# Performance work log

Measured on AMD Instinct MI355X. Metric: run time of the kernel, lower is better.

## Reference

```python
import jax, jax.numpy as jnp
import numpy as np

MAX_DEGREE = 5
NUM_LAYERS = 2


def setup_inputs() -> dict:
    key = jax.random.key(0)
    ks = jax.random.split(key, 10)
    N, F, H, C, E = 200000, 128, 64, 40, 3200000
    x = jax.random.normal(ks[0], (N, F), dtype=jnp.float32)
    edge_index = jax.random.randint(ks[1], (2, E), 0, N, dtype=jnp.int32)
    # torch Linear init ~ U(-1/sqrt(fan_in), 1/sqrt(fan_in)); scaled normals are fine for a baseline
    W1 = jax.random.normal(ks[2], (F, H), dtype=jnp.float32) / np.sqrt(F)
    b1 = jax.random.normal(ks[3], (H,), dtype=jnp.float32) * 0.01
    relW = jax.random.normal(ks[4], (NUM_LAYERS, MAX_DEGREE + 1, H, H), dtype=jnp.float32) / np.sqrt(H)
    relb = jax.random.normal(ks[5], (NUM_LAYERS, MAX_DEGREE + 1, H), dtype=jnp.float32) * 0.01
    Wout = jax.random.normal(ks[6], (H, C), dtype=jnp.float32) / np.sqrt(H)
    bout = jax.random.normal(ks[7], (C,), dtype=jnp.float32) * 0.01
    fuse = jnp.full((NUM_LAYERS,), 1.0 / (NUM_LAYERS + 1), dtype=jnp.float32)
    return {"x": x, "edge_index": edge_index, "W1": W1, "b1": b1,
            "relW": relW, "relb": relb, "Wout": Wout, "bout": bout, "fuse": fuse}


def reference(x, edge_index, W1, b1, relW, relb, Wout, bout, fuse):
    N = x.shape[0]
    src, dst = edge_index[0], edge_index[1]
    loop_mask = (src != dst)  # remove_self_loops
    # degree on target nodes (flow='source_to_target'), clamped to max_degree
    deg = jax.ops.segment_sum(loop_mask.astype(jnp.int32), dst, num_segments=N)
    deg = jnp.clip(deg, 0, MAX_DEGREE)
    node_idx = jnp.arange(N)

    h = jax.nn.relu(x @ W1 + b1)  # dropout is identity in eval mode
    x_first = h
    for i in range(NUM_LAYERS):
        # scatter-add aggregation; self loops added back (root_weight=False)
        msg = jnp.where(loop_mask[:, None], h[src], 0.0)  # [E, H]
        agg = jax.ops.segment_sum(msg, dst, num_segments=N) + h  # [N, H]
        # degree-bucketed linear: compute all 6 buckets, select per node
        all_out = jnp.einsum('nd,kdo->kno', agg, relW[i]) + relb[i][:, None, :]  # [6, N, H]
        conv = all_out[deg, node_idx]  # [N, H]
        h = conv + fuse[i] * x_first
    logits = h @ Wout + bout
    return jax.nn.log_softmax(logits, axis=-1)
```

## Files before the change

kernel.cpp:

```cpp
#include <hip/hip_runtime.h>
#include <cmath>
#include <cstddef>

#define F_IN 128
#define H_DIM 64
#define C_OUT 40
#define MAXDEG 5
#define EPB 16

typedef __attribute__((ext_vector_type(8))) _Float16 half8;
typedef __attribute__((ext_vector_type(4))) _Float16 half4;
typedef __attribute__((ext_vector_type(4))) float fv4;
typedef __attribute__((ext_vector_type(2))) float fv2;

__device__ __forceinline__ half4 u2h(uint2 u) { return __builtin_bit_cast(half4, u); }
__device__ __forceinline__ uint2 h2u(half4 v) { return __builtin_bit_cast(uint2, v); }
__device__ __forceinline__ half8 u2h8(uint4 u) { return __builtin_bit_cast(half8, u); }
__device__ __forceinline__ uint4 h2u8(half8 v) { return __builtin_bit_cast(uint4, v); }


__global__ __launch_bounds__(256) void k_scatter(const int* __restrict__ src,
                                                 const int* __restrict__ dst,
                                                 int E, int NB, int stride,
                                                 int* __restrict__ gcnt,
                                                 unsigned int* __restrict__ ebuf) {
    __shared__ int hist[512];
    __shared__ int base[512];
    int tid = threadIdx.x;
    for (int i = tid; i < NB; i += 256) hist[i] = 0;
    __syncthreads();
    int e0 = blockIdx.x * (256 * EPB);
    int es[EPB], ed[EPB];
#pragma unroll
    for (int i = 0; i < EPB; ++i) {
        int e = e0 + i * 256 + tid;
        int s = -1, d = -1;
        if (e < E) { s = src[e]; d = dst[e]; }
        es[i] = s; ed[i] = d;
        if (d >= 0 && s != d) atomicAdd(&hist[d >> 9], 1);
    }
    __syncthreads();
    for (int i = tid; i < NB; i += 256) {
        int c = hist[i];
        base[i] = c ? atomicAdd(&gcnt[i], c) : 0;
        hist[i] = 0;
    }
    __syncthreads();
#pragma unroll
    for (int i = 0; i < EPB; ++i) {
        int s = es[i], d = ed[i];
        if (d >= 0 && s != d) {
            int b = d >> 9;
            int p = base[b] + atomicAdd(&hist[b], 1);
            if (p < stride)
                ebuf[(size_t)b * stride + p] = ((unsigned)(d & 511) << 20) | (unsigned)s;
        }
    }
}

__global__ __launch_bounds__(512) void k_build(const unsigned int* __restrict__ ebuf,
                                               const int* __restrict__ gcnt, int stride, int N,
                                               int* __restrict__ row, int* __restrict__ cnt,
                                               int* __restrict__ col) {
    __shared__ int lcnt[512];
    __shared__ int lcur[512];
    int bk = blockIdx.x;
    int n0 = bk << 9;
    int tid = threadIdx.x;
    int ebase = bk * stride;
    int ec = min(gcnt[bk], stride);
    int eend = ebase + ec;
    lcnt[tid] = 0;
    __syncthreads();
    for (int e = ebase + tid; e < eend; e += 512)
        atomicAdd(&lcnt[ebuf[e] >> 20], 1);
    __syncthreads();
    int v = lcnt[tid];
    lcur[tid] = v;
    __syncthreads();
    for (int off = 1; off < 512; off <<= 1) {
        int t = (tid >= off) ? lcur[tid - off] : 0;
        __syncthreads();
        lcur[tid] += t;
        __syncthreads();
    }
    int ex = lcur[tid] - v;
    __syncthreads();
    lcur[tid] = ebase + ex;
    int n = n0 + tid;
    if (n < N) {
        row[n] = ebase + ex;
        cnt[n] = v;
    }
    __syncthreads();
    for (int e = ebase + tid; e < eend; e += 512) {
        unsigned edv = ebuf[e];
        int dl = edv >> 20;
        int p = atomicAdd(&lcur[dl], 1);
        col[p] = (int)(edv & 0xFFFFF);
    }
}

__global__ __launch_bounds__(256) void k_lin1(const float* __restrict__ x,
                                              const float* __restrict__ W1,
                                              const float* __restrict__ b1,
                                              _Float16* __restrict__ h,
                                              _Float16* __restrict__ hz2,
                                              unsigned char* __restrict__ hq,
                                              unsigned char* __restrict__ hq2,
                                              int N, int ngroups) {
    __shared__ _Float16 Wl[4 * 4 * 64 * 8];
    int tid = threadIdx.x;
    if (blockIdx.x == 0) {
        if (tid < 64) {
            h[(size_t)N * H_DIM + tid] = (_Float16)0.f;
            hz2[(size_t)N * H_DIM + tid] = (_Float16)0.f;
        }
        if (tid < 16) {
            ((unsigned*)(hq + (size_t)N * 64))[tid] = 0u;
            ((unsigned*)(hq2 + (size_t)N * 64))[tid] = 0u;
        }
    }
    for (int idx = tid; idx < 4 * 4 * 64 * 8; idx += 256) {
        int j = idx & 7, ln = (idx >> 3) & 63, ks = (idx >> 9) & 3, t = idx >> 11;
        int k = ks * 32 + (ln >> 4) * 8 + j;
        int n = t * 16 + (ln & 15);
        Wl[idx] = (_Float16)W1[k * H_DIM + n];
    }
    __syncthreads();

    int wave = tid >> 6, lane = tid & 63;
    int m = lane & 15, quad = lane >> 4;

    fv4 bb[4];
#pragma unroll
    for (int t = 0; t < 4; ++t)
        bb[t] = *(const fv4*)(b1 + t * 16 + quad * 4);

    auto loadx = [&](int gg, half8* dst) {
        int row = gg * 64 + wave * 16 + m;
        int rc = (row < N) ? row : (N - 1);
        const float* xr = x + (size_t)rc * F_IN + quad * 8;
#pragma unroll
        for (int ks = 0; ks < 4; ++ks) {
            fv4 lo = *(const fv4*)(xr + ks * 32);
            fv4 hi = *(const fv4*)(xr + ks * 32 + 4);
            half8 av;
#pragma unroll
            for (int j = 0; j < 4; ++j) av[j] = (_Float16)lo[j];
#pragma unroll
            for (int j = 0; j < 4; ++j) av[4 + j] = (_Float16)hi[j];
            dst[ks] = av;
        }
    };

    int g = blockIdx.x;
    half8 a[4];
    if (g < ngroups) loadx(g, a);
    while (g < ngroups) {
        int gn = g + gridDim.x;
        half8 an[4];
        if (gn < ngroups) loadx(gn, an);

        fv4 acc[4];
#pragma unroll
        for (int t = 0; t < 4; ++t) acc[t] = (fv4){0.f, 0.f, 0.f, 0.f};
#pragma unroll
        for (int ks = 0; ks < 4; ++ks) {
#pragma unroll
            for (int t = 0; t < 4; ++t) {
                half8 b = *(const half8*)&Wl[(((t * 4 + ks) * 64) + lane) * 8];
                acc[t] = __builtin_amdgcn_mfma_f32_16x16x32_f16(b, a[ks], acc[t], 0, 0, 0);
            }
        }
        int row = g * 64 + wave * 16 + m;
        if (row < N) {
            _Float16* hr = h + (size_t)row * H_DIM;
            unsigned* hqr = (unsigned*)(hq) + (size_t)row * 16;
#pragma unroll
            for (int t = 0; t < 4; ++t) {
                float f[4];
                half4 hv;
#pragma unroll
                for (int reg = 0; reg < 4; ++reg) {
                    f[reg] = fmaxf(acc[t][reg] + bb[t][reg], 0.f);
                    hv[reg] = (_Float16)f[reg];
                }
                *reinterpret_cast<half4*>(hr + t * 16 + quad * 4) = hv;
                int q = __builtin_amdgcn_cvt_pk_fp8_f32(f[0], f[1], 0, 0);
                q = __builtin_amdgcn_cvt_pk_fp8_f32(f[2], f[3], q, 1);
                hqr[t * 4 + quad] = (unsigned)q;
            }
        }
#pragma unroll
        for (int ks = 0; ks < 4; ++ks) a[ks] = an[ks];
        g = gn;
    }
}

__global__ void k_agg(const _Float16* __restrict__ hin,
                      const unsigned char* __restrict__ hq,
                      const int* __restrict__ row,
                      const int* __restrict__ cnt, const int* __restrict__ col,
                      _Float16* __restrict__ agg, int N) {
    int wid = (blockIdx.x * blockDim.x + threadIdx.x) >> 6;
    int lane = threadIdx.x & 63;
    int g = lane >> 3, fl = lane & 7, gl = g << 3;
    int n = wid * 8 + g;
    bool nv = (n < N);
    int nn = nv ? n : (N - 1);
    int base = row[nn];
    int c = nv ? cnt[nn] : 0;
    const uint2* hv8 = (const uint2*)hq;
    int cmax = c;
    cmax = max(cmax, __shfl_xor(cmax, 8));
    cmax = max(cmax, __shfl_xor(cmax, 16));
    cmax = max(cmax, __shfl_xor(cmax, 32));
    float acc[8] = {0.f, 0.f, 0.f, 0.f, 0.f, 0.f, 0.f, 0.f};
    for (int j0 = 0; j0 < cmax; j0 += 8) {
        int idx = j0 + fl;
        int myc = (idx < c) ? col[base + idx] : N;
        int tmax = min(8, cmax - j0);
        if (tmax == 8) {
            uint2 u[8];
#pragma unroll
            for (int t = 0; t < 8; ++t) {
                int s = __shfl(myc, gl + t);
                u[t] = hv8[(size_t)s * 8 + fl];
            }
#pragma unroll
            for (int t = 0; t < 8; ++t) {
                fv2 p0 = __builtin_amdgcn_cvt_pk_f32_fp8((int)u[t].x, 0);
                fv2 p1 = __builtin_amdgcn_cvt_pk_f32_fp8((int)u[t].x, 1);
                fv2 p2 = __builtin_amdgcn_cvt_pk_f32_fp8((int)u[t].y, 0);
                fv2 p3 = __builtin_amdgcn_cvt_pk_f32_fp8((int)u[t].y, 1);
                acc[0] += p0[0]; acc[1] += p0[1]; acc[2] += p1[0]; acc[3] += p1[1];
                acc[4] += p2[0]; acc[5] += p2[1]; acc[6] += p3[0]; acc[7] += p3[1];
            }
        } else {
            for (int t = 0; t < tmax; ++t) {
                int s = __shfl(myc, gl + t);
                uint2 u = hv8[(size_t)s * 8 + fl];
                fv2 p0 = __builtin_amdgcn_cvt_pk_f32_fp8((int)u.x, 0);
                fv2 p1 = __builtin_amdgcn_cvt_pk_f32_fp8((int)u.x, 1);
                fv2 p2 = __builtin_amdgcn_cvt_pk_f32_fp8((int)u.y, 0);
                fv2 p3 = __builtin_amdgcn_cvt_pk_f32_fp8((int)u.y, 1);
                acc[0] += p0[0]; acc[1] += p0[1]; acc[2] += p1[0]; acc[3] += p1[1];
                acc[4] += p2[0]; acc[5] += p2[1]; acc[6] += p3[0]; acc[7] += p3[1];
            }
        }
    }
    const uint4* hv16 = (const uint4*)hin;
    half8 sh = u2h8(hv16[(size_t)nn * 8 + fl]);
#pragma unroll
    for (int i = 0; i < 8; ++i) acc[i] += (float)sh[i];
    if (nv) {
        half8 o;
#pragma unroll
        for (int i = 0; i < 8; ++i) o[i] = (_Float16)acc[i];
        ((uint4*)agg)[(size_t)nn * 8 + fl] = h2u8(o);
    }
}

__global__ __launch_bounds__(256) void k_bucket(const _Float16* __restrict__ agg,
                                                const int* __restrict__ cnt,
                                                const float* __restrict__ relW,
                                                const float* __restrict__ relb,
                                                const float* __restrict__ fuse, int layer,
                                                const _Float16* __restrict__ xfirst,
                                                _Float16* __restrict__ h,
                                                unsigned char* __restrict__ hq, int N) {
    __shared__ _Float16 Wl[4 * 2 * 64 * 8];
    __shared__ int flist[64];
    __shared__ int fn;
    const float* W = relW + (size_t)(layer * 6 + MAXDEG) * (H_DIM * H_DIM);
    int tid = threadIdx.x;
    if (tid == 0) fn = 0;
    for (int idx = tid; idx < 4 * 2 * 64 * 8; idx += 256) {
        int j = idx & 7, ln = (idx >> 3) & 63, ks = (idx >> 9) & 1, t = idx >> 10;
        int k = ks * 32 + (ln >> 4) * 8 + j;
        int n = t * 16 + (ln & 15);
        Wl[idx] = (_Float16)W[k * H_DIM + n];
    }
    __syncthreads();

    int wave = tid >> 6, lane = tid & 63;
    int row0 = blockIdx.x * 64 + wave * 16;
    int m = lane & 15, quad = lane >> 4;
    int row = row0 + m;
    int rc = (row < N) ? row : (N - 1);
    float fu = fuse[layer];
    const float* bias = relb + (layer * 6 + MAXDEG) * H_DIM;

    half8 a[2];
#pragma unroll
    for (int ks = 0; ks < 2; ++ks)
        a[ks] = *(const half8*)(agg + (size_t)rc * H_DIM + ks * 32 + quad * 8);

    fv4 acc[4];
#pragma unroll
    for (int t = 0; t < 4; ++t) acc[t] = (fv4){0.f, 0.f, 0.f, 0.f};
#pragma unroll
    for (int ks = 0; ks < 2; ++ks)
#pragma unroll
        for (int t = 0; t < 4; ++t) {
            half8 b = *(const half8*)&Wl[(((t * 2 + ks) * 64) + lane) * 8];
            acc[t] = __builtin_amdgcn_mfma_f32_16x16x32_f16(b, a[ks], acc[t], 0, 0, 0);
        }

    int c = (row < N) ? cnt[row] : MAXDEG;
    if (quad == 0 && row < N && c < MAXDEG) {
        int p = atomicAdd(&fn, 1);
        if (p < 64) flist[p] = wave * 16 + m;
    }
    if (row < N && c >= MAXDEG) {
        _Float16* hr = h + (size_t)row * H_DIM;
        unsigned* hqr = (unsigned*)(hq) + (size_t)row * 16;
        const _Float16* xr = xfirst + (size_t)row * H_DIM;
#pragma unroll
        for (int t = 0; t < 4; ++t) {
            fv4 bv = *(const fv4*)(bias + t * 16 + quad * 4);
            half4 xf = *reinterpret_cast<const half4*>(xr + t * 16 + quad * 4);
            float f[4];
            half4 hvv;
#pragma unroll
            for (int reg = 0; reg < 4; ++reg) {
                f[reg] = acc[t][reg] + bv[reg] + fu * (float)xf[reg];
                hvv[reg] = (_Float16)f[reg];
            }
            *reinterpret_cast<half4*>(hr + t * 16 + quad * 4) = hvv;
            int q = __builtin_amdgcn_cvt_pk_fp8_f32(f[0], f[1], 0, 0);
            q = __builtin_amdgcn_cvt_pk_fp8_f32(f[2], f[3], q, 1);
            hqr[t * 4 + quad] = (unsigned)q;
        }
    }
    __syncthreads();
    int M = min(fn, 64);
    for (int i = wave; i < M; i += 4) {
        int rl = flist[i];
        int r = blockIdx.x * 64 + rl;
        int d = cnt[r];
        const float* Wd = relW + (size_t)(layer * 6 + d) * (H_DIM * H_DIM);
        float av = (float)agg[(size_t)r * H_DIM + lane];
        float accf = relb[(layer * 6 + d) * H_DIM + lane];
        for (int k = 0; k < 64; ++k)
            accf = fmaf(__shfl(av, k), Wd[k * H_DIM + lane], accf);
        accf += fu * (float)xfirst[(size_t)r * H_DIM + lane];
        h[(size_t)r * H_DIM + lane] = (_Float16)accf;
        float a0 = __shfl(accf, lane & ~1);
        float a1 = __shfl(accf, lane | 1);
        if (!(lane & 1)) {
            int q = __builtin_amdgcn_cvt_pk_fp8_f32(a0, a1, 0, 0);
            ((unsigned short*)(hq + (size_t)r * 64))[lane >> 1] = (unsigned short)(q & 0xFFFF);
        }
    }
}

#define HB 80
__global__ __launch_bounds__(256) void k_bucket_out(const _Float16* __restrict__ agg,
                                                    const int* __restrict__ cnt,
                                                    const float* __restrict__ relW,
                                                    const float* __restrict__ relb,
                                                    const float* __restrict__ fuse,
                                                    const _Float16* __restrict__ xfirst,
                                                    const float* __restrict__ Wout,
                                                    const float* __restrict__ bout,
                                                    float* __restrict__ out, int N) {
    __shared__ _Float16 Wl[4 * 2 * 64 * 8];
    __shared__ _Float16 Wo[3 * 2 * 64 * 8];
    __shared__ _Float16 hbuf[64 * HB];
    __shared__ int flist[64];
    __shared__ int fn;
    const int layer = 1;
    const float* W = relW + (size_t)(layer * 6 + MAXDEG) * (H_DIM * H_DIM);
    int tid = threadIdx.x;
    if (tid == 0) fn = 0;
    for (int idx = tid; idx < 4 * 2 * 64 * 8; idx += 256) {
        int j = idx & 7, ln = (idx >> 3) & 63, ks = (idx >> 9) & 1, t = idx >> 10;
        int k = ks * 32 + (ln >> 4) * 8 + j;
        int n = t * 16 + (ln & 15);
        Wl[idx] = (_Float16)W[k * H_DIM + n];
    }
    for (int idx = tid; idx < 3 * 2 * 64 * 8; idx += 256) {
        int j = idx & 7, ln = (idx >> 3) & 63, ks = (idx >> 9) & 1, t = idx >> 10;
        int k = ks * 32 + (ln >> 4) * 8 + j;
        int n = t * 16 + (ln & 15);
        Wo[idx] = (n < C_OUT) ? (_Float16)Wout[k * C_OUT + n] : (_Float16)0.f;
    }
    __syncthreads();

    int wave = tid >> 6, lane = tid & 63;
    int row0 = blockIdx.x * 64 + wave * 16;
    int m = lane & 15, quad = lane >> 4;
    int row = row0 + m;
    int rc = (row < N) ? row : (N - 1);
    float fu = fuse[layer];
    const float* bias = relb + (layer * 6 + MAXDEG) * H_DIM;

    half8 a[2];
#pragma unroll
    for (int ks = 0; ks < 2; ++ks)
        a[ks] = *(const half8*)(agg + (size_t)rc * H_DIM + ks * 32 + quad * 8);

    fv4 acc[4];
#pragma unroll
    for (int t = 0; t < 4; ++t) acc[t] = (fv4){0.f, 0.f, 0.f, 0.f};
#pragma unroll
    for (int ks = 0; ks < 2; ++ks)
#pragma unroll
        for (int t = 0; t < 4; ++t) {
            half8 b = *(const half8*)&Wl[(((t * 2 + ks) * 64) + lane) * 8];
            acc[t] = __builtin_amdgcn_mfma_f32_16x16x32_f16(b, a[ks], acc[t], 0, 0, 0);
        }

    int c = (row < N) ? cnt[row] : MAXDEG;
    if (quad == 0 && row < N && c < MAXDEG) {
        int p = atomicAdd(&fn, 1);
        if (p < 64) flist[p] = wave * 16 + m;
    }
    {
        int rl = wave * 16 + m;
        const _Float16* xr = xfirst + (size_t)rc * H_DIM;
#pragma unroll
        for (int t = 0; t < 4; ++t) {
            fv4 bv = *(const fv4*)(bias + t * 16 + quad * 4);
            half4 xf = *reinterpret_cast<const half4*>(xr + t * 16 + quad * 4);
            half4 hvv;
#pragma unroll
            for (int reg = 0; reg < 4; ++reg)
                hvv[reg] = (_Float16)(acc[t][reg] + bv[reg] + fu * (float)xf[reg]);
            *reinterpret_cast<half4*>(&hbuf[rl * HB + t * 16 + quad * 4]) = hvv;
        }
    }
    __syncthreads();
    int M = min(fn, 64);
    for (int i = wave; i < M; i += 4) {
        int rl = flist[i];
        int r = blockIdx.x * 64 + rl;
        int d = cnt[r];
        const float* Wd = relW + (size_t)(layer * 6 + d) * (H_DIM * H_DIM);
        float av = (float)agg[(size_t)r * H_DIM + lane];
        float accf = relb[(layer * 6 + d) * H_DIM + lane];
        for (int k = 0; k < 64; ++k)
            accf = fmaf(__shfl(av, k), Wd[k * H_DIM + lane], accf);
        accf += fu * (float)xfirst[(size_t)r * H_DIM + lane];
        hbuf[rl * HB + lane] = (_Float16)accf;
    }
    __syncthreads();

    half8 ao[2];
#pragma unroll
    for (int ks = 0; ks < 2; ++ks)
        ao[ks] = *(const half8*)&hbuf[(wave * 16 + m) * HB + ks * 32 + quad * 8];

    fv4 lacc[3];
#pragma unroll
    for (int t = 0; t < 3; ++t) lacc[t] = (fv4){0.f, 0.f, 0.f, 0.f};
#pragma unroll
    for (int ks = 0; ks < 2; ++ks)
#pragma unroll
        for (int t = 0; t < 3; ++t) {
            half8 b = *(const half8*)&Wo[(((t * 2 + ks) * 64) + lane) * 8];
            lacc[t] = __builtin_amdgcn_mfma_f32_16x16x32_f16(ao[ks], b, lacc[t], 0, 0, 0);
        }
    bool v2 = (m < 8);
    float b0 = bout[m], b1v = bout[16 + m], b2v = v2 ? bout[32 + m] : 0.f;
#pragma unroll
    for (int reg = 0; reg < 4; ++reg) {
        int r = row0 + quad * 4 + reg;
        float l0 = lacc[0][reg] + b0;
        float l1 = lacc[1][reg] + b1v;
        float l2 = v2 ? (lacc[2][reg] + b2v) : -INFINITY;
        float mx = fmaxf(fmaxf(l0, l1), l2);
#pragma unroll
        for (int off = 1; off < 16; off <<= 1) mx = fmaxf(mx, __shfl_xor(mx, off));
        float s = expf(l0 - mx) + expf(l1 - mx) + (v2 ? expf(l2 - mx) : 0.f);
#pragma unroll
        for (int off = 1; off < 16; off <<= 1) s += __shfl_xor(s, off);
        float ls = logf(s);
        if (r < N) {
            out[(size_t)r * C_OUT + m] = l0 - mx - ls;
            out[(size_t)r * C_OUT + 16 + m] = l1 - mx - ls;
            if (v2) out[(size_t)r * C_OUT + 32 + m] = l2 - mx - ls;
        }
    }
}

extern "C" void kernel_launch(void* const* d_in, const int* in_sizes, int n_in,
                              void* d_out, int out_size, void* d_ws, size_t ws_size,
                              hipStream_t stream) {
    const float* x    = (const float*)d_in[0];
    const int*   ei   = (const int*)d_in[1];
    const float* W1   = (const float*)d_in[2];
    const float* b1   = (const float*)d_in[3];
    const float* relW = (const float*)d_in[4];
    const float* relb = (const float*)d_in[5];
    const float* Wout = (const float*)d_in[6];
    const float* bout = (const float*)d_in[7];
    const float* fuse = (const float*)d_in[8];
    float* out = (float*)d_out;

    int N = in_sizes[0] / F_IN;
    int E = in_sizes[1] / 2;
    const int* src = ei;
    const int* dst = ei + E;
    int NB = (N + 511) >> 9;
    int mean = (E + NB - 1) / NB;
    int stride = mean + mean / 8 + 512;

    char* w = (char*)d_ws;
    auto alloc = [&](size_t bytes) {
        char* p = w;
        w += (bytes + 255) & ~(size_t)255;
        return p;
    };
    int* cnt  = (int*)alloc((size_t)N * 4);
    int* row  = (int*)alloc((size_t)N * 4);
    int* gcnt = (int*)alloc(1024 * 4);
    int* col  = (int*)alloc((size_t)NB * stride * 4);
    _Float16* h0   = (_Float16*)alloc((size_t)(N + 1) * H_DIM * 2);
    _Float16* h1   = (_Float16*)alloc((size_t)(N + 1) * H_DIM * 2);
    _Float16* aggb = (_Float16*)alloc((size_t)N * H_DIM * 2);
    unsigned char* h0q = (unsigned char*)alloc((size_t)(N + 1) * 64);
    unsigned char* h1q = (unsigned char*)alloc((size_t)(N + 1) * 64);
    unsigned int* ebuf = (unsigned int*)h0;

    hipMemsetAsync(gcnt, 0, 1024 * 4, stream);

    k_scatter<<<(E + 256 * EPB - 1) / (256 * EPB), 256, 0, stream>>>(src, dst, E, NB, stride, gcnt, ebuf);
    k_build<<<NB, 512, 0, stream>>>(ebuf, gcnt, stride, N, row, cnt, col);

    int tiles = (N + 15) / 16;
    int gblk = (tiles + 3) / 4;
    int awaves = (N + 7) / 8;
    int ablk = (awaves * 64 + 255) / 256;

    int ngroups = (N + 63) / 64;
    int lblk = ngroups < 2048 ? ngroups : 2048;
    k_lin1<<<lblk, 256, 0, stream>>>(x, W1, b1, h0, h1, h0q, h1q, N, ngroups);

    k_agg<<<ablk, 256, 0, stream>>>(h0, h0q, row, cnt, col, aggb, N);
    k_bucket<<<gblk, 256, 0, stream>>>(aggb, cnt, relW, relb, fuse, 0, h0, h1, h1q, N);

    k_agg<<<ablk, 256, 0, stream>>>(h1, h1q, row, cnt, col, aggb, N);
    k_bucket_out<<<gblk, 256, 0, stream>>>(aggb, cnt, relW, relb, fuse, h0, Wout, bout, out, N);
}
```

Measured before the change: 442.7 us.

## Merge edge scatter and first linear layer into one horizontally fused launch

Combines the edge bucketing scatter kernel and the first dense layer (x@W1) into a single launch, with block-index ranges choosing which role each block plays. The two independent stages can then run at the same time on the GPU, overlapping memory-bound scatter work with the MFMA GEMM and removing one launch. Because they now run concurrently, ebuf gets its own workspace allocation instead of aliasing h0. The lin1 grid is also capped at 1024 blocks instead of 2048.

```diff
diff --git a/kernel.cpp b/kernel.cpp
--- a/kernel.cpp
+++ b/kernel.cpp
@@ -18,43 +18,140 @@
 __device__ __forceinline__ half8 u2h8(uint4 u) { return __builtin_bit_cast(half8, u); }
 __device__ __forceinline__ uint4 h2u8(half8 v) { return __builtin_bit_cast(uint4, v); }
 
-
-__global__ __launch_bounds__(256) void k_scatter(const int* __restrict__ src,
-                                                 const int* __restrict__ dst,
-                                                 int E, int NB, int stride,
-                                                 int* __restrict__ gcnt,
-                                                 unsigned int* __restrict__ ebuf) {
-    __shared__ int hist[512];
-    __shared__ int base[512];
+__global__ __launch_bounds__(256) void k_scatter_lin1(
+        const int* __restrict__ src, const int* __restrict__ dst,
+        int E, int NB, int stride, int* __restrict__ gcnt,
+        unsigned int* __restrict__ ebuf, int SB,
+        const float* __restrict__ x, const float* __restrict__ W1,
+        const float* __restrict__ b1,
+        _Float16* __restrict__ h, _Float16* __restrict__ hz2,
+        unsigned char* __restrict__ hq, unsigned char* __restrict__ hq2,
+        int N, int ngroups) {
+    __shared__ __align__(16) unsigned char smem_raw[16384];
     int tid = threadIdx.x;
-    for (int i = tid; i < NB; i += 256) hist[i] = 0;
-    __syncthreads();
-    int e0 = blockIdx.x * (256 * EPB);
-    int es[EPB], ed[EPB];
-#pragma unroll
-    for (int i = 0; i < EPB; ++i) {
-        int e = e0 + i * 256 + tid;
-        int s = -1, d = -1;
-        if (e < E) { s = src[e]; d = dst[e]; }
-        es[i] = s; ed[i] = d;
-        if (d >= 0 && s != d) atomicAdd(&hist[d >> 9], 1);
-    }
-    __syncthreads();
-    for (int i = tid; i < NB; i += 256) {
-        int c = hist[i];
-        base[i] = c ? atomicAdd(&gcnt[i], c) : 0;
-        hist[i] = 0;
-    }
-    __syncthreads();
-#pragma unroll
-    for (int i = 0; i < EPB; ++i) {
-        int s = es[i], d = ed[i];
-        if (d >= 0 && s != d) {
-            int b = d >> 9;
-            int p = base[b] + atomicAdd(&hist[b], 1);
-            if (p < stride)
-                ebuf[(size_t)b * stride + p] = ((unsigned)(d & 511) << 20) | (unsigned)s;
-        }
+
+    if (blockIdx.x < SB) {
+        int* hist = (int*)smem_raw;
+        int* base = (int*)(smem_raw + 2048);
+        for (int i = tid; i < NB; i += 256) hist[i] = 0;
+        __syncthreads();
+        int e0 = blockIdx.x * (256 * EPB);
+        int es[EPB], ed[EPB];
+#pragma unroll
+        for (int i = 0; i < EPB; ++i) {
+            int e = e0 + i * 256 + tid;
+            int s = -1, d = -1;
+            if (e < E) { s = src[e]; d = dst[e]; }
+            es[i] = s; ed[i] = d;
+            if (d >= 0 && s != d) atomicAdd(&hist[d >> 9], 1);
+        }
+        __syncthreads();
+        for (int i = tid; i < NB; i += 256) {
+            int c = hist[i];
+            base[i] = c ? atomicAdd(&gcnt[i], c) : 0;
+            hist[i] = 0;
+        }
+        __syncthreads();
+#pragma unroll
+        for (int i = 0; i < EPB; ++i) {
+            int s = es[i], d = ed[i];
+            if (d >= 0 && s != d) {
+                int b = d >> 9;
+                int p = base[b] + atomicAdd(&hist[b], 1);
+                if (p < stride)
+                    ebuf[(size_t)b * stride + p] = ((unsigned)(d & 511) << 20) | (unsigned)s;
+            }
+        }
+        return;
+    }
+
+    _Float16* Wl = (_Float16*)smem_raw;
+    int lb = blockIdx.x - SB;
+    int LG = gridDim.x - SB;
+    if (lb == 0) {
+        if (tid < 64) {
+            h[(size_t)N * H_DIM + tid] = (_Float16)0.f;
+            hz2[(size_t)N * H_DIM + tid] = (_Float16)0.f;
+        }
+        if (tid < 16) {
+            ((unsigned*)(hq + (size_t)N * 64))[tid] = 0u;
+            ((unsigned*)(hq2 + (size_t)N * 64))[tid] = 0u;
+        }
+    }
+    for (int idx = tid; idx < 4 * 4 * 64 * 8; idx += 256) {
+        int j = idx & 7, ln = (idx >> 3) & 63, ks = (idx >> 9) & 3, t = idx >> 11;
+        int k = ks * 32 + (ln >> 4) * 8 + j;
+        int n = t * 16 + (ln & 15);
+        Wl[idx] = (_Float16)W1[k * H_DIM + n];
+    }
+    __syncthreads();
+
+    int wave = tid >> 6, lane = tid & 63;
+    int m = lane & 15, quad = lane >> 4;
+
+    fv4 bb[4];
+#pragma unroll
+    for (int t = 0; t < 4; ++t)
+        bb[t] = *(const fv4*)(b1 + t * 16 + quad * 4);
+
+    auto loadx = [&](int gg, half8* dstv) {
+        int row = gg * 64 + wave * 16 + m;
+        int rc = (row < N) ? row : (N - 1);
+        const float* xr = x + (size_t)rc * F_IN + quad * 8;
+#pragma unroll
+        for (int ks = 0; ks < 4; ++ks) {
+            fv4 lo = *(const fv4*)(xr + ks * 32);
+            fv4 hi = *(const fv4*)(xr + ks * 32 + 4);
+            half8 av;
+#pragma unroll
+            for (int j = 0; j < 4; ++j) av[j] = (_Float16)lo[j];
+#pragma unroll
+            for (int j = 0; j < 4; ++j) av[4 + j] = (_Float16)hi[j];
+            dstv[ks] = av;
+        }
+    };
+
+    int g = lb;
+    half8 a[4];
+    if (g < ngroups) loadx(g, a);
+    while (g < ngroups) {
+        int gn = g + LG;
+        half8 an[4];
+        if (gn < ngroups) loadx(gn, an);
+
+        fv4 acc[4];
+#pragma unroll
+        for (int t = 0; t < 4; ++t) acc[t] = (fv4){0.f, 0.f, 0.f, 0.f};
+#pragma unroll
+        for (int ks = 0; ks < 4; ++ks) {
+#pragma unroll
+            for (int t = 0; t < 4; ++t) {
+                half8 b = *(const half8*)&Wl[(((t * 4 + ks) * 64) + lane) * 8];
+                acc[t] = __builtin_amdgcn_mfma_f32_16x16x32_f16(b, a[ks], acc[t], 0, 0, 0);
+            }
+        }
+        int row = g * 64 + wave * 16 + m;
+        if (row < N) {
+            _Float16* hr = h + (size_t)row * H_DIM;
+            unsigned* hqr = (unsigned*)(hq) + (size_t)row * 16;
+#pragma unroll
+            for (int t = 0; t < 4; ++t) {
+                float f[4];
+                half4 hv;
+#pragma unroll
+                for (int reg = 0; reg < 4; ++reg) {
+                    f[reg] = fmaxf(acc[t][reg] + bb[t][reg], 0.f);
+                    hv[reg] = (_Float16)f[reg];
+                }
+                *reinterpret_cast<half4*>(hr + t * 16 + quad * 4) = hv;
+                int q = __builtin_amdgcn_cvt_pk_fp8_f32(f[0], f[1], 0, 0);
+                q = __builtin_amdgcn_cvt_pk_fp8_f32(f[2], f[3], q, 1);
+                hqr[t * 4 + quad] = (unsigned)q;
+            }
+        }
+#pragma unroll
+        for (int ks = 0; ks < 4; ++ks) a[ks] = an[ks];
+        g = gn;
     }
 }
 
@@ -98,103 +195,6 @@
         int dl = edv >> 20;
         int p = atomicAdd(&lcur[dl], 1);
         col[p] = (int)(edv & 0xFFFFF);
-    }
-}
-
-__global__ __launch_bounds__(256) void k_lin1(const float* __restrict__ x,
-                                              const float* __restrict__ W1,
-                                              const float* __restrict__ b1,
-                                              _Float16* __restrict__ h,
-                                              _Float16* __restrict__ hz2,
-                                              unsigned char* __restrict__ hq,
-                                              unsigned char* __restrict__ hq2,
-                                              int N, int ngroups) {
-    __shared__ _Float16 Wl[4 * 4 * 64 * 8];
-    int tid = threadIdx.x;
-    if (blockIdx.x == 0) {
-        if (tid < 64) {
-            h[(size_t)N * H_DIM + tid] = (_Float16)0.f;
-            hz2[(size_t)N * H_DIM + tid] = (_Float16)0.f;
-        }
-        if (tid < 16) {
-            ((unsigned*)(hq + (size_t)N * 64))[tid] = 0u;
-            ((unsigned*)(hq2 + (size_t)N * 64))[tid] = 0u;
-        }
-    }
-    for (int idx = tid; idx < 4 * 4 * 64 * 8; idx += 256) {
-        int j = idx & 7, ln = (idx >> 3) & 63, ks = (idx >> 9) & 3, t = idx >> 11;
-        int k = ks * 32 + (ln >> 4) * 8 + j;
-        int n = t * 16 + (ln & 15);
-        Wl[idx] = (_Float16)W1[k * H_DIM + n];
-    }
-    __syncthreads();
-
-    int wave = tid >> 6, lane = tid & 63;
-    int m = lane & 15, quad = lane >> 4;
-
-    fv4 bb[4];
-#pragma unroll
-    for (int t = 0; t < 4; ++t)
-        bb[t] = *(const fv4*)(b1 + t * 16 + quad * 4);
-
-    auto loadx = [&](int gg, half8* dst) {
-        int row = gg * 64 + wave * 16 + m;
-        int rc = (row < N) ? row : (N - 1);
-        const float* xr = x + (size_t)rc * F_IN + quad * 8;
-#pragma unroll
-        for (int ks = 0; ks < 4; ++ks) {
-            fv4 lo = *(const fv4*)(xr + ks * 32);
-            fv4 hi = *(const fv4*)(xr + ks * 32 + 4);
-            half8 av;
-#pragma unroll
-            for (int j = 0; j < 4; ++j) av[j] = (_Float16)lo[j];
-#pragma unroll
-            for (int j = 0; j < 4; ++j) av[4 + j] = (_Float16)hi[j];
-            dst[ks] = av;
-        }
-    };
-
-    int g = blockIdx.x;
-    half8 a[4];
-    if (g < ngroups) loadx(g, a);
-    while (g < ngroups) {
-        int gn = g + gridDim.x;
-        half8 an[4];
-        if (gn < ngroups) loadx(gn, an);
-
-        fv4 acc[4];
-#pragma unroll
-        for (int t = 0; t < 4; ++t) acc[t] = (fv4){0.f, 0.f, 0.f, 0.f};
-#pragma unroll
-        for (int ks = 0; ks < 4; ++ks) {
-#pragma unroll
-            for (int t = 0; t < 4; ++t) {
-                half8 b = *(const half8*)&Wl[(((t * 4 + ks) * 64) + lane) * 8];
-                acc[t] = __builtin_amdgcn_mfma_f32_16x16x32_f16(b, a[ks], acc[t], 0, 0, 0);
-            }
-        }
-        int row = g * 64 + wave * 16 + m;
-        if (row < N) {
-            _Float16* hr = h + (size_t)row * H_DIM;
-            unsigned* hqr = (unsigned*)(hq) + (size_t)row * 16;
-#pragma unroll
-            for (int t = 0; t < 4; ++t) {
-                float f[4];
-                half4 hv;
-#pragma unroll
-                for (int reg = 0; reg < 4; ++reg) {
-                    f[reg] = fmaxf(acc[t][reg] + bb[t][reg], 0.f);
-                    hv[reg] = (_Float16)f[reg];
-                }
-                *reinterpret_cast<half4*>(hr + t * 16 + quad * 4) = hv;
-                int q = __builtin_amdgcn_cvt_pk_fp8_f32(f[0], f[1], 0, 0);
-                q = __builtin_amdgcn_cvt_pk_fp8_f32(f[2], f[3], q, 1);
-                hqr[t * 4 + quad] = (unsigned)q;
-            }
-        }
-#pragma unroll
-        for (int ks = 0; ks < 4; ++ks) a[ks] = an[ks];
-        g = gn;
     }
 }
 
@@ -523,11 +523,16 @@
     _Float16* aggb = (_Float16*)alloc((size_t)N * H_DIM * 2);
     unsigned char* h0q = (unsigned char*)alloc((size_t)(N + 1) * 64);
     unsigned char* h1q = (unsigned char*)alloc((size_t)(N + 1) * 64);
-    unsigned int* ebuf = (unsigned int*)h0;
+    unsigned int* ebuf = (unsigned int*)alloc((size_t)NB * stride * 4);
 
     hipMemsetAsync(gcnt, 0, 1024 * 4, stream);
 
-    k_scatter<<<(E + 256 * EPB - 1) / (256 * EPB), 256, 0, stream>>>(src, dst, E, NB, stride, gcnt, ebuf);
+    int sblk = (E + 256 * EPB - 1) / (256 * EPB);
+    int ngroups = (N + 63) / 64;
+    int lgrid = ngroups < 1024 ? ngroups : 1024;
+    k_scatter_lin1<<<sblk + lgrid, 256, 0, stream>>>(src, dst, E, NB, stride, gcnt, ebuf,
+                                                     sblk, x, W1, b1, h0, h1, h0q, h1q,
+                                                     N, ngroups);
     k_build<<<NB, 512, 0, stream>>>(ebuf, gcnt, stride, N, row, cnt, col);
 
     int tiles = (N + 15) / 16;
@@ -535,10 +540,6 @@
     int awaves = (N + 7) / 8;
     int ablk = (awaves * 64 + 255) / 256;
 
-    int ngroups = (N + 63) / 64;
-    int lblk = ngroups < 2048 ? ngroups : 2048;
-    k_lin1<<<lblk, 256, 0, stream>>>(x, W1, b1, h0, h1, h0q, h1q, N, ngroups);
-
     k_agg<<<ablk, 256, 0, stream>>>(h0, h0q, row, cnt, col, aggb, N);
     k_bucket<<<gblk, 256, 0, stream>>>(aggb, cnt, relW, relb, fuse, 0, h0, h1, h1q, N);
 
```

After: 434.9 us. No clear change (-1.8%).
